# Kernel tuning notes

Measured on AMD Instinct MI355X. Metric: run time of the kernel, lower is better.

Reference implementation:

```python
import jax, jax.numpy as jnp
import numpy as np

# PyTorch LSTM cell with zero initial (h, c): W_hh @ h0 == 0, and c = sigmoid(i)*tanh(g)
# since the forget-gate term f*c0 vanishes. Gate order in torch: i, f, g, o.
# b here is the combined b_ih + b_hh (identical math).

def lstm_step0(x, Wih, b):
    pre = x @ Wih.T + b                      # (N, 4H)
    i, f, g, o = jnp.split(pre, 4, axis=-1)
    c = jax.nn.sigmoid(i) * jnp.tanh(g)
    return jax.nn.sigmoid(o) * jnp.tanh(c)   # (N, H)


def setup_inputs() -> dict:
    key = jax.random.key(0)
    ks = jax.random.split(key, 13)
    num_ts, num_periods, F = 128, 256, 128
    GH, NH, NF = 512, 256, 10
    s = lambda k, shape, fan: (jax.random.normal(k, shape, jnp.float32) / np.sqrt(fan))
    return {
        "X": jax.random.normal(ks[0], (num_ts, num_periods, F), jnp.float32),
        "g_Wih0": s(ks[1], (4 * GH, F), F),
        "g_b0": s(ks[2], (4 * GH,), GH),
        "g_Wih1": s(ks[3], (4 * GH, GH), GH),
        "g_b1": s(ks[4], (4 * GH,), GH),
        "aff_W": s(ks[5], (NF, GH), GH),
        "aff_b": s(ks[6], (NF,), GH),
        "n_Wih0": s(ks[7], (4 * NH, F), F),
        "n_b0": s(ks[8], (4 * NH,), NH),
        "n_Wih1": s(ks[9], (4 * NH, NH), NH),
        "n_b1": s(ks[10], (4 * NH,), NH),
        "noise_W": s(ks[11], (1, NH), NH),
        "noise_b": s(ks[12], (1,), NH),
    }


def reference(X, g_Wih0, g_b0, g_Wih1, g_b1, aff_W, aff_b,
              n_Wih0, n_b0, n_Wih1, n_b1, noise_W, noise_b):
    num_ts, num_periods, num_feats = X.shape
    x = X.reshape(-1, num_feats)             # (num_ts*num_periods, F)

    # Global factor branch: 2-layer LSTM single step from zero state
    hg = lstm_step0(lstm_step0(x, g_Wih0, g_b0), g_Wih1, g_b1)
    hg = jax.nn.relu(hg)
    mus = (hg @ aff_W.T + aff_b).sum(axis=-1).reshape(num_ts, num_periods)

    # Noise branch: 2-layer LSTM single step from zero state
    hn = lstm_step0(lstm_step0(x, n_Wih0, n_b0), n_Wih1, n_b1)
    hn = jax.nn.relu(hn)
    sigmas = jax.nn.softplus(hn @ noise_W.T + noise_b)  # log(1+exp(.)), stable
    sigmas = sigmas.reshape(num_ts, num_periods) + 1e-6
    return mus, sigmas
```

## Files before the change

### kernel.cpp

```cpp
#include <hip/hip_runtime.h>
#include <hip/hip_bf16.h>
#include <hip/hip_fp16.h>

typedef _Float16 h8_t __attribute__((ext_vector_type(8)));
typedef _Float16 h4_t __attribute__((ext_vector_type(4)));
typedef float f4_t __attribute__((ext_vector_type(4)));

#define M_ROWS 32768

__device__ __forceinline__ void gload_lds16(const void* g, void* l) {
  __builtin_amdgcn_global_load_lds((const __attribute__((address_space(1))) void*)g,
                                   (__attribute__((address_space(3))) void*)l, 16, 0, 0);
}

__device__ __forceinline__ float sigmoid_f(float x) { return 1.f / (1.f + __expf(-x)); }
__device__ __forceinline__ float tanh_f(float x) { return 1.f - 2.f / (__expf(2.f * x) + 1.f); }

struct GArgs {
  const _Float16* A;
  const _Float16* W;
  const float* bias;
  _Float16* Hout;
  const float* rvec;
  float* partial;
};

__global__ void prep_all(const float* __restrict__ X, const float* __restrict__ gW0,
                         const float* __restrict__ gW1, const float* __restrict__ nW0,
                         const float* __restrict__ nW1, const float* __restrict__ aff_W,
                         const float* __restrict__ aff_b,
                         _Float16* __restrict__ Xh, _Float16* __restrict__ Wg0,
                         _Float16* __restrict__ Wg1, _Float16* __restrict__ Wn0,
                         _Float16* __restrict__ Wn1,
                         float* __restrict__ pg, float* __restrict__ pn,
                         float* __restrict__ wsum) {
  int b = blockIdx.x;
  const float* s; _Float16* d; int base;
  if (b < 4096)      { s = X;   d = Xh;  base = b; }
  else if (b < 4352) { s = gW0; d = Wg0; base = b - 4096; }
  else if (b < 5376) { s = gW1; d = Wg1; base = b - 4352; }
  else if (b < 5504) { s = nW0; d = Wn0; base = b - 5376; }
  else if (b < 5760) { s = nW1; d = Wn1; base = b - 5504; }
  else if (b < 5888) {
    int i = (b - 5760) * 256 + threadIdx.x;
    pg[i] = 0.f; pn[i] = 0.f;
    return;
  } else {
    int j = (b - 5888) * 256 + threadIdx.x;
    float sum = 0.f;
#pragma unroll
    for (int r = 0; r < 10; ++r) sum += aff_W[r * 512 + j];
    wsum[j] = sum;
    if (j == 0) {
      float bs = 0.f;
#pragma unroll
      for (int r = 0; r < 10; ++r) bs += aff_b[r];
      wsum[512] = bs;
    }
    return;
  }
  int i4 = (base * 256 + threadIdx.x) * 4;
  float4 v = *(const float4*)(s + i4);
  h4_t o;
  o[0] = (_Float16)v.x; o[1] = (_Float16)v.y; o[2] = (_Float16)v.z; o[3] = (_Float16)v.w;
  *(h4_t*)(d + i4) = o;
}

template <int K_DIM, int H_DIM, bool FUSE>
__device__ __forceinline__ void gemm_body(const GArgs& ga, int h0,
                                          _Float16* As, _Float16* Bs) {
  const int tid = threadIdx.x;
  const int wid = tid >> 6;
  const int lane = tid & 63;
  const int wave_m = wid >> 1;
  const int wave_h = wid & 1;
  const int q = lane >> 4;
  const int tcol = lane & 15;
  const int m0 = blockIdx.x * 128;

  const _Float16* aptr[4]; int aoff[4];
#pragma unroll
  for (int c = 0; c < 4; ++c) {
    int o = ((wid * 4 + c) << 10) + (lane << 4);
    int row = o >> 7, pch = (o >> 4) & 7;
    int lch = pch ^ (row & 7);
    aptr[c] = ga.A + (size_t)(m0 + row) * K_DIM + lch * 8;
    aoff[c] = o;
  }
  const _Float16* bptr[6]; int boff[6];
#pragma unroll
  for (int c = 0; c < 6; ++c) {
    int o = ((wid * 6 + c) << 10) + (lane << 4);
    int pan = o >> 13;
    int row = (o >> 7) & 63, pch = (o >> 4) & 7;
    int lch = pch ^ (row & 7);
    int gbase = (pan == 0 ? 0 : (pan == 1 ? 2 * H_DIM : 3 * H_DIM)) + h0 + row;
    bptr[c] = ga.W + (size_t)gbase * K_DIM + lch * 8;
    boff[c] = o;
  }
  int a_rd[2][4];
#pragma unroll
  for (int ks = 0; ks < 2; ++ks)
#pragma unroll
    for (int mi = 0; mi < 4; ++mi) {
      int r = wave_m * 64 + mi * 16 + tcol;
      int c = ks * 4 + q;
      a_rd[ks][mi] = r * 64 + (c ^ (r & 7)) * 8;
    }
  int b_rd[2][2];
#pragma unroll
  for (int ks = 0; ks < 2; ++ks)
#pragma unroll
    for (int ni = 0; ni < 2; ++ni) {
      int j = wave_h * 32 + ni * 16 + tcol;
      int c = ks * 4 + q;
      b_rd[ks][ni] = j * 64 + (c ^ (j & 7)) * 8;
    }

  f4_t acc[3][4][2];
#pragma unroll
  for (int p = 0; p < 3; ++p)
#pragma unroll
    for (int mi = 0; mi < 4; ++mi)
#pragma unroll
      for (int ni = 0; ni < 2; ++ni) acc[p][mi][ni] = (f4_t){0.f, 0.f, 0.f, 0.f};

#pragma unroll
  for (int kk = 0; kk < K_DIM / 64; ++kk) {
#pragma unroll
    for (int c = 0; c < 4; ++c) gload_lds16(aptr[c], (char*)As + aoff[c]);
#pragma unroll
    for (int c = 0; c < 6; ++c) gload_lds16(bptr[c], (char*)Bs + boff[c]);
#pragma unroll
    for (int c = 0; c < 4; ++c) aptr[c] += 64;
#pragma unroll
    for (int c = 0; c < 6; ++c) bptr[c] += 64;
    __syncthreads();

#pragma unroll
    for (int ks = 0; ks < 2; ++ks) {
      h8_t af[4];
#pragma unroll
      for (int mi = 0; mi < 4; ++mi) af[mi] = *(const h8_t*)&As[a_rd[ks][mi]];
#pragma unroll
      for (int p = 0; p < 3; ++p) {
#pragma unroll
        for (int ni = 0; ni < 2; ++ni) {
          h8_t bf = *(const h8_t*)&Bs[p * 4096 + b_rd[ks][ni]];
#pragma unroll
          for (int mi = 0; mi < 4; ++mi)
            acc[p][mi][ni] = __builtin_amdgcn_mfma_f32_16x16x32_f16(af[mi], bf, acc[p][mi][ni], 0, 0, 0);
        }
      }
    }
    __syncthreads();
  }

  const int mrow0 = m0 + wave_m * 64;
  const int jcol0 = h0 + wave_h * 32;

  if constexpr (!FUSE) {
#pragma unroll
    for (int ni = 0; ni < 2; ++ni) {
      int j = jcol0 + ni * 16 + tcol;
      float bi = ga.bias[j];
      float bg = ga.bias[2 * H_DIM + j];
      float bo = ga.bias[3 * H_DIM + j];
#pragma unroll
      for (int mi = 0; mi < 4; ++mi)
#pragma unroll
        for (int r = 0; r < 4; ++r) {
          float pi = acc[0][mi][ni][r] + bi;
          float pgt = acc[1][mi][ni][r] + bg;
          float po = acc[2][mi][ni][r] + bo;
          float cc = sigmoid_f(pi) * tanh_f(pgt);
          float hh = sigmoid_f(po) * tanh_f(cc);
          int m = mrow0 + mi * 16 + q * 4 + r;
          ga.Hout[(size_t)m * H_DIM + j] = (_Float16)hh;
        }
    }
  } else {
    float rsum[4][4];
#pragma unroll
    for (int mi = 0; mi < 4; ++mi)
#pragma unroll
      for (int r = 0; r < 4; ++r) rsum[mi][r] = 0.f;
#pragma unroll
    for (int ni = 0; ni < 2; ++ni) {
      int j = jcol0 + ni * 16 + tcol;
      float bi = ga.bias[j];
      float bg = ga.bias[2 * H_DIM + j];
      float bo = ga.bias[3 * H_DIM + j];
      float rv = ga.rvec[j];
#pragma unroll
      for (int mi = 0; mi < 4; ++mi)
#pragma unroll
        for (int r = 0; r < 4; ++r) {
          float pi = acc[0][mi][ni][r] + bi;
          float pgt = acc[1][mi][ni][r] + bg;
          float po = acc[2][mi][ni][r] + bo;
          float cc = sigmoid_f(pi) * tanh_f(pgt);
          float hh = sigmoid_f(po) * tanh_f(cc);
          hh = fmaxf(hh, 0.f);
          rsum[mi][r] += hh * rv;
        }
    }
#pragma unroll
    for (int mi = 0; mi < 4; ++mi)
#pragma unroll
      for (int r = 0; r < 4; ++r) {
        float v = rsum[mi][r];
        v += __shfl_xor(v, 1);
        v += __shfl_xor(v, 2);
        v += __shfl_xor(v, 4);
        v += __shfl_xor(v, 8);
        if (tcol == 0) atomicAdd(&ga.partial[mrow0 + mi * 16 + q * 4 + r], v);
      }
  }
}

__global__ __launch_bounds__(256, 2) void layer1_fused(GArgs g, GArgs n) {
  __shared__ __align__(16) _Float16 As[128 * 64];
  __shared__ __align__(16) _Float16 Bs[3 * 64 * 64];
  int y = blockIdx.y;
  if (y < 8) gemm_body<128, 512, false>(g, y * 64, As, Bs);
  else       gemm_body<128, 256, false>(n, (y - 8) * 64, As, Bs);
}

__global__ __launch_bounds__(256, 2) void layer2_fused(GArgs g, GArgs n) {
  __shared__ __align__(16) _Float16 As[128 * 64];
  __shared__ __align__(16) _Float16 Bs[3 * 64 * 64];
  int y = blockIdx.y;
  if (y < 8) gemm_body<512, 512, true>(g, y * 64, As, Bs);
  else       gemm_body<256, 256, true>(n, (y - 8) * 64, As, Bs);
}

__global__ void finalize(const float* __restrict__ pg, const float* __restrict__ pn,
                         const float* __restrict__ wsum, const float* __restrict__ noise_b,
                         float* __restrict__ out) {
  int i = blockIdx.x * blockDim.x + threadIdx.x;
  out[i] = pg[i] + wsum[512];
  float x = pn[i] + noise_b[0];
  float sp = fmaxf(x, 0.f) + log1pf(expf(-fabsf(x)));
  out[M_ROWS + i] = sp + 1e-6f;
}

extern "C" void kernel_launch(void* const* d_in, const int* in_sizes, int n_in,
                              void* d_out, int out_size, void* d_ws, size_t ws_size,
                              hipStream_t stream) {
  const float* X       = (const float*)d_in[0];
  const float* g_Wih0  = (const float*)d_in[1];
  const float* g_b0    = (const float*)d_in[2];
  const float* g_Wih1  = (const float*)d_in[3];
  const float* g_b1    = (const float*)d_in[4];
  const float* aff_W   = (const float*)d_in[5];
  const float* aff_b   = (const float*)d_in[6];
  const float* n_Wih0  = (const float*)d_in[7];
  const float* n_b0    = (const float*)d_in[8];
  const float* n_Wih1  = (const float*)d_in[9];
  const float* n_b1    = (const float*)d_in[10];
  const float* noise_W = (const float*)d_in[11];
  const float* noise_b = (const float*)d_in[12];
  float* out = (float*)d_out;

  char* w = (char*)d_ws;
  _Float16* Xh  = (_Float16*)w; w += (size_t)M_ROWS * 128 * 2;
  _Float16* Wg0 = (_Float16*)w; w += 2048 * 128 * 2;
  _Float16* Wg1 = (_Float16*)w; w += 2048 * 512 * 2;
  _Float16* Wn0 = (_Float16*)w; w += 1024 * 128 * 2;
  _Float16* Wn1 = (_Float16*)w; w += 1024 * 256 * 2;
  _Float16* h1g = (_Float16*)w; w += (size_t)M_ROWS * 512 * 2;
  _Float16* h1n = (_Float16*)w; w += (size_t)M_ROWS * 256 * 2;
  float* pg   = (float*)w; w += (size_t)M_ROWS * 4;
  float* pn   = (float*)w; w += (size_t)M_ROWS * 4;
  float* wsum = (float*)w; w += 4096;

  prep_all<<<5890, 256, 0, stream>>>(X, g_Wih0, g_Wih1, n_Wih0, n_Wih1, aff_W, aff_b,
                                     Xh, Wg0, Wg1, Wn0, Wn1, pg, pn, wsum);

  GArgs l1g = {Xh, Wg0, g_b0, h1g, nullptr, nullptr};
  GArgs l1n = {Xh, Wn0, n_b0, h1n, nullptr, nullptr};
  layer1_fused<<<dim3(M_ROWS / 128, 12), 256, 0, stream>>>(l1g, l1n);

  GArgs l2g = {h1g, Wg1, g_b1, nullptr, wsum, pg};
  GArgs l2n = {h1n, Wn1, n_b1, nullptr, noise_W, pn};
  layer2_fused<<<dim3(M_ROWS / 128, 12), 256, 0, stream>>>(l2g, l2n);

  finalize<<<M_ROWS / 256, 256, 0, stream>>>(pg, pn, wsum, noise_b, out);
}
```

Measured before the change: 262.8 us.

## Double-buffer A tiles in LDS and load weight fragments directly into registers

Weight (B) operands no longer go through shared memory. Each lane loads its MFMA B fragments straight from global memory into registers and prefetches the next K-step's fragments. The A tile is double-buffered in LDS so the next tile's global-to-LDS copy overlaps the current MFMAs, leaving one barrier per iteration instead of two. This removes the B LDS staging and a sync, but adds register pressure from the two fragment sets and uncoalesced per-lane global reads of the weights.

```diff
diff --git a/kernel.cpp b/kernel.cpp
--- a/kernel.cpp
+++ b/kernel.cpp
@@ -67,8 +67,7 @@
 }
 
 template <int K_DIM, int H_DIM, bool FUSE>
-__device__ __forceinline__ void gemm_body(const GArgs& ga, int h0,
-                                          _Float16* As, _Float16* Bs) {
+__device__ __forceinline__ void gemm_body(const GArgs& ga, int h0, _Float16* As) {
   const int tid = threadIdx.x;
   const int wid = tid >> 6;
   const int lane = tid & 63;
@@ -77,6 +76,7 @@
   const int q = lane >> 4;
   const int tcol = lane & 15;
   const int m0 = blockIdx.x * 128;
+  constexpr int NK = K_DIM / 64;
 
   const _Float16* aptr[4]; int aoff[4];
 #pragma unroll
@@ -87,17 +87,6 @@
     aptr[c] = ga.A + (size_t)(m0 + row) * K_DIM + lch * 8;
     aoff[c] = o;
   }
-  const _Float16* bptr[6]; int boff[6];
-#pragma unroll
-  for (int c = 0; c < 6; ++c) {
-    int o = ((wid * 6 + c) << 10) + (lane << 4);
-    int pan = o >> 13;
-    int row = (o >> 7) & 63, pch = (o >> 4) & 7;
-    int lch = pch ^ (row & 7);
-    int gbase = (pan == 0 ? 0 : (pan == 1 ? 2 * H_DIM : 3 * H_DIM)) + h0 + row;
-    bptr[c] = ga.W + (size_t)gbase * K_DIM + lch * 8;
-    boff[c] = o;
-  }
   int a_rd[2][4];
 #pragma unroll
   for (int ks = 0; ks < 2; ++ks)
@@ -107,53 +96,75 @@
       int c = ks * 4 + q;
       a_rd[ks][mi] = r * 64 + (c ^ (r & 7)) * 8;
     }
-  int b_rd[2][2];
+
+  const _Float16* Wb[3][2];
+#pragma unroll
+  for (int ni = 0; ni < 2; ++ni) {
+    Wb[0][ni] = ga.W + (size_t)(0 * H_DIM + ni * 16) * K_DIM;
+    Wb[1][ni] = ga.W + (size_t)(2 * H_DIM + ni * 16) * K_DIM;
+    Wb[2][ni] = ga.W + (size_t)(3 * H_DIM + ni * 16) * K_DIM;
+  }
+  int rk = (h0 + wave_h * 32 + tcol) * K_DIM + q * 8;
+
+  f4_t acc[3][4][2];
+#pragma unroll
+  for (int p = 0; p < 3; ++p)
+#pragma unroll
+    for (int mi = 0; mi < 4; ++mi)
+#pragma unroll
+      for (int ni = 0; ni < 2; ++ni) acc[p][mi][ni] = (f4_t){0.f, 0.f, 0.f, 0.f};
+
+  h8_t bf_cur[2][3][2], bf_next[2][3][2];
+#pragma unroll
+  for (int c = 0; c < 4; ++c) gload_lds16(aptr[c], (char*)As + aoff[c]);
 #pragma unroll
   for (int ks = 0; ks < 2; ++ks)
 #pragma unroll
-    for (int ni = 0; ni < 2; ++ni) {
-      int j = wave_h * 32 + ni * 16 + tcol;
-      int c = ks * 4 + q;
-      b_rd[ks][ni] = j * 64 + (c ^ (j & 7)) * 8;
-    }
-
-  f4_t acc[3][4][2];
-#pragma unroll
-  for (int p = 0; p < 3; ++p)
-#pragma unroll
-    for (int mi = 0; mi < 4; ++mi)
-#pragma unroll
-      for (int ni = 0; ni < 2; ++ni) acc[p][mi][ni] = (f4_t){0.f, 0.f, 0.f, 0.f};
-
-#pragma unroll
-  for (int kk = 0; kk < K_DIM / 64; ++kk) {
-#pragma unroll
-    for (int c = 0; c < 4; ++c) gload_lds16(aptr[c], (char*)As + aoff[c]);
-#pragma unroll
-    for (int c = 0; c < 6; ++c) gload_lds16(bptr[c], (char*)Bs + boff[c]);
-#pragma unroll
-    for (int c = 0; c < 4; ++c) aptr[c] += 64;
-#pragma unroll
-    for (int c = 0; c < 6; ++c) bptr[c] += 64;
+    for (int p = 0; p < 3; ++p)
+#pragma unroll
+      for (int ni = 0; ni < 2; ++ni)
+        bf_cur[ks][p][ni] = *(const h8_t*)(Wb[p][ni] + rk + ks * 32);
+
+#pragma unroll
+  for (int kk = 0; kk < NK; ++kk) {
     __syncthreads();
 
+    if (kk + 1 < NK) {
+#pragma unroll
+      for (int c = 0; c < 4; ++c)
+        gload_lds16(aptr[c] + (kk + 1) * 64, (char*)As + (((kk + 1) & 1) << 14) + aoff[c]);
+      int rkn = rk + (kk + 1) * 64;
+#pragma unroll
+      for (int ks = 0; ks < 2; ++ks)
+#pragma unroll
+        for (int p = 0; p < 3; ++p)
+#pragma unroll
+          for (int ni = 0; ni < 2; ++ni)
+            bf_next[ks][p][ni] = *(const h8_t*)(Wb[p][ni] + rkn + ks * 32);
+    }
+
+    const _Float16* Ab = As + ((kk & 1) << 13);
 #pragma unroll
     for (int ks = 0; ks < 2; ++ks) {
       h8_t af[4];
 #pragma unroll
-      for (int mi = 0; mi < 4; ++mi) af[mi] = *(const h8_t*)&As[a_rd[ks][mi]];
-#pragma unroll
-      for (int p = 0; p < 3; ++p) {
-#pragma unroll
-        for (int ni = 0; ni < 2; ++ni) {
-          h8_t bf = *(const h8_t*)&Bs[p * 4096 + b_rd[ks][ni]];
+      for (int mi = 0; mi < 4; ++mi) af[mi] = *(const h8_t*)&Ab[a_rd[ks][mi]];
+#pragma unroll
+      for (int p = 0; p < 3; ++p)
+#pragma unroll
+        for (int ni = 0; ni < 2; ++ni)
 #pragma unroll
           for (int mi = 0; mi < 4; ++mi)
-            acc[p][mi][ni] = __builtin_amdgcn_mfma_f32_16x16x32_f16(af[mi], bf, acc[p][mi][ni], 0, 0, 0);
-        }
-      }
-    }
-    __syncthreads();
+            acc[p][mi][ni] = __builtin_amdgcn_mfma_f32_16x16x32_f16(af[mi], bf_cur[ks][p][ni], acc[p][mi][ni], 0, 0, 0);
+    }
+    if (kk + 1 < NK) {
+#pragma unroll
+      for (int ks = 0; ks < 2; ++ks)
+#pragma unroll
+        for (int p = 0; p < 3; ++p)
+#pragma unroll
+          for (int ni = 0; ni < 2; ++ni) bf_cur[ks][p][ni] = bf_next[ks][p][ni];
+    }
   }
 
   const int mrow0 = m0 + wave_m * 64;
@@ -220,19 +231,17 @@
 }
 
 __global__ __launch_bounds__(256, 2) void layer1_fused(GArgs g, GArgs n) {
-  __shared__ __align__(16) _Float16 As[128 * 64];
-  __shared__ __align__(16) _Float16 Bs[3 * 64 * 64];
+  __shared__ __align__(16) _Float16 As[2 * 128 * 64];
   int y = blockIdx.y;
-  if (y < 8) gemm_body<128, 512, false>(g, y * 64, As, Bs);
-  else       gemm_body<128, 256, false>(n, (y - 8) * 64, As, Bs);
+  if (y < 8) gemm_body<128, 512, false>(g, y * 64, As);
+  else       gemm_body<128, 256, false>(n, (y - 8) * 64, As);
 }
 
 __global__ __launch_bounds__(256, 2) void layer2_fused(GArgs g, GArgs n) {
-  __shared__ __align__(16) _Float16 As[128 * 64];
-  __shared__ __align__(16) _Float16 Bs[3 * 64 * 64];
+  __shared__ __align__(16) _Float16 As[2 * 128 * 64];
   int y = blockIdx.y;
-  if (y < 8) gemm_body<512, 512, true>(g, y * 64, As, Bs);
-  else       gemm_body<256, 256, true>(n, (y - 8) * 64, As, Bs);
+  if (y < 8) gemm_body<512, 512, true>(g, y * 64, As);
+  else       gemm_body<256, 256, true>(n, (y - 8) * 64, As);
 }
 
 __global__ void finalize(const float* __restrict__ pg, const float* __restrict__ pn,
```

Result: slower. 316.9 us (+20.6%).
